# Optimization experiments

Hardware: AMD Instinct MI355X
Metric: run time of the kernel (lower is better)

## Reference

```python
import jax, jax.numpy as jnp
import numpy as np

N = 50000   # nodes
E = 800000  # edges
B = 64      # graphs in batch
IN = 128    # in_features
HID = 64    # hidden_channels
H = 4       # head_count
C = 10      # out_classes
NEG = 0.2   # leaky relu negative slope
EPS = 1e-5  # batchnorm eps (eval mode, running mean 0 / var 1)


def _gat(x, edge_index, W, a_src, a_dst, b):
    """PyG GATConv (add_self_loops=False, concat=True), eval mode (no dropout)."""
    Hh, F = a_src.shape
    xW = (x @ W).reshape(-1, Hh, F)                       # [N,H,F]
    src, dst = edge_index[0], edge_index[1]
    e = (jnp.einsum('nhf,hf->nh', xW, a_src)[src]
         + jnp.einsum('nhf,hf->nh', xW, a_dst)[dst])      # [E,H]
    e = jnp.where(e > 0, e, NEG * e)                      # leaky relu
    m = jax.ops.segment_max(e, dst, num_segments=N)       # per-dst max
    m = jnp.where(jnp.isfinite(m), m, 0.0)
    p = jnp.exp(e - m[dst])
    denom = jax.ops.segment_sum(p, dst, num_segments=N)
    alpha = p / jnp.maximum(denom[dst], 1e-16)            # edge softmax over dst
    out = jax.ops.segment_sum(alpha[:, :, None] * xW[src], dst, num_segments=N)
    return out.reshape(-1, Hh * F) + b


def _bn_relu(y, g, be):
    # BatchNorm1d in eval mode with running_mean=0, running_var=1, then ReLU
    return jax.nn.relu(g * y / jnp.sqrt(1.0 + EPS) + be)


def setup_inputs():
    key = jax.random.key(0)
    ks = jax.random.split(key, 24)
    s = lambda k, shape: (jax.random.normal(k, shape, jnp.float32) * 0.05)
    z = lambda shape: jnp.zeros(shape, jnp.float32)
    o = lambda shape: jnp.ones(shape, jnp.float32)
    return {
        'acc_flag': 0,
        'x': jax.random.normal(ks[0], (N, IN), jnp.float32),
        'edge_index': jax.random.randint(ks[1], (2, E), 0, N),
        'batch': jnp.sort(jax.random.randint(ks[2], (N,), 0, B)),
        # layer 1: GATConv(IN -> HID, heads=H, concat)
        'W1': s(ks[3], (IN, H * HID)), 'a_src1': s(ks[4], (H, HID)), 'a_dst1': s(ks[5], (H, HID)), 'b1': z((H * HID,)),
        # proj: GATConv(H*HID -> HID, heads=1) + BN
        'W2': s(ks[6], (H * HID, HID)), 'a_src2': s(ks[7], (1, HID)), 'a_dst2': s(ks[8], (1, HID)), 'b2': z((HID,)), 'g2': o((HID,)), 'be2': z((HID,)),
        # block 1
        'W3': s(ks[9], (HID, HID)), 'a_src3': s(ks[10], (1, HID)), 'a_dst3': s(ks[11], (1, HID)), 'b3': z((HID,)), 'g3': o((HID,)), 'be3': z((HID,)),
        # block 2
        'W4': s(ks[12], (HID, HID)), 'a_src4': s(ks[13], (1, HID)), 'a_dst4': s(ks[14], (1, HID)), 'b4': z((HID,)), 'g4': o((HID,)), 'be4': z((HID,)),
        # MLP head
        'Wh1': s(ks[15], (HID, 128)), 'bh1': z((128,)),
        'Wh2': s(ks[16], (128, C)), 'bh2': z((C,)),
    }


def reference(acc_flag, x, edge_index, batch,
              W1, a_src1, a_dst1, b1,
              W2, a_src2, a_dst2, b2, g2, be2,
              W3, a_src3, a_dst3, b3, g3, be3,
              W4, a_src4, a_dst4, b4, g4, be4,
              Wh1, bh1, Wh2, bh2):
    # hardware GAT layer + ReLU (relu applied twice in original -> idempotent)
    x1 = jax.nn.relu(_gat(x, edge_index, W1, a_src1, a_dst1, b1))   # [N, H*HID]
    # projection block: residual base is zeros (shape mismatch H*HID vs HID)
    h = _bn_relu(_gat(x1, edge_index, W2, a_src2, a_dst2, b2), g2, be2)
    # residual blocks (shapes match -> x + relu(bn(y)))
    h = h + _bn_relu(_gat(h, edge_index, W3, a_src3, a_dst3, b3), g3, be3)
    h = h + _bn_relu(_gat(h, edge_index, W4, a_src4, a_dst4, b4), g4, be4)
    # global mean pool over graphs
    pooled = jax.ops.segment_sum(h, batch, num_segments=B)
    cnt = jnp.maximum(jax.ops.segment_sum(jnp.ones((N,), h.dtype), batch, num_segments=B), 1.0)
    hp = pooled / cnt[:, None]                                      # [B, HID]
    # MLP head
    return jax.nn.relu(hp @ Wh1 + bh1) @ Wh2 + bh2                  # [B, C]
```

## Files before the change

### kernel.cpp

```cpp
#include <hip/hip_runtime.h>

#define N_NODES 50000
#define N_EDGES 800000
#define N_GRAPHS 64
#define NEG_SLOPE 0.2f
#define BN_RSQ 0.9999950000374997f
#define NB_SCAN ((N_NODES + 255) / 256)

typedef __bf16 bf16x8 __attribute__((ext_vector_type(8)));
typedef float floatx4 __attribute__((ext_vector_type(4)));

__device__ __forceinline__ float lrelu(float v) { return v > 0.0f ? v : NEG_SLOPE * v; }

__device__ __forceinline__ float b2f(unsigned short u) {
    return __uint_as_float(((unsigned int)u) << 16);
}
__device__ __forceinline__ unsigned short f2b(float f) {
    unsigned int u = __float_as_uint(f);
    return (unsigned short)((u + 0x7fffu + ((u >> 16) & 1u)) >> 16);
}
__device__ __forceinline__ float blo(unsigned int d) { return __uint_as_float(d << 16); }
__device__ __forceinline__ float bhi(unsigned int d) { return __uint_as_float(d & 0xffff0000u); }

__global__ void k_prep(const int* __restrict__ ei, int* __restrict__ deg,
                       const float* __restrict__ W1, const float* __restrict__ W2,
                       const float* __restrict__ W3, const float* __restrict__ W4,
                       unsigned short* __restrict__ Wt1, unsigned short* __restrict__ Wt2,
                       unsigned short* __restrict__ Wt3, unsigned short* __restrict__ Wt4) {
    int i = blockIdx.x * 256 + threadIdx.x;
    if (i < 32768) {
        int k = i >> 8, n = i & 255;
        Wt1[n * 128 + k] = f2b(W1[i]);
    } else if (i < 49152) {
        int j = i - 32768;
        int k = j >> 6, n = j & 63;
        Wt2[n * 256 + k] = f2b(W2[j]);
    } else if (i < 53248) {
        int j = i - 49152;
        int k = j >> 6, n = j & 63;
        Wt3[n * 64 + k] = f2b(W3[j]);
    } else if (i < 57344) {
        int j = i - 53248;
        int k = j >> 6, n = j & 63;
        Wt4[n * 64 + k] = f2b(W4[j]);
    }
    if (i < N_EDGES) atomicAdd(&deg[ei[N_EDGES + i]], 1);
}

__global__ __launch_bounds__(256) void k_offs(const int* __restrict__ deg, int* __restrict__ offs,
                                              int* __restrict__ total, const int* __restrict__ batch,
                                              int* __restrict__ bounds, int* __restrict__ bh) {
    __shared__ int lh[64];
    if (threadIdx.x < 64) lh[threadIdx.x] = 0;
    __syncthreads();
    if (blockIdx.x == 0 && threadIdx.x <= N_GRAPHS) {
        int g = threadIdx.x;
        int lo = 0, hi = N_NODES;
        while (lo < hi) {
            int mid = (lo + hi) >> 1;
            if (batch[mid] < g) lo = mid + 1; else hi = mid;
        }
        bounds[g] = lo;
    }
    int i = blockIdx.x * blockDim.x + threadIdx.x;
    int lane = threadIdx.x & 63;
    int v = (i < N_NODES) ? deg[i] : 0;
    int incl = v;
    for (int o = 1; o < 64; o <<= 1) {
        int t = __shfl_up(incl, o);
        if (lane >= o) incl += t;
    }
    int wtot = __shfl(incl, 63);
    int base = 0;
    if (lane == 0) base = atomicAdd(total, wtot);
    base = __shfl(base, 0);
    if (i < N_NODES) {
        offs[i] = base + incl - v;
        atomicAdd(&lh[63 - min(v, 63)], 1);
    }
    __syncthreads();
    if (threadIdx.x < 64) bh[blockIdx.x * 64 + threadIdx.x] = lh[threadIdx.x];
}

__global__ __launch_bounds__(256) void k_pscan(const int* __restrict__ bh, int* __restrict__ bb) {
    __shared__ int partial[4][64];
    __shared__ int bbase[64];
    const int tid = threadIdx.x;
    const int b = tid & 63, q = tid >> 6;
    const int per = (NB_SCAN + 3) / 4;
    const int k0 = q * per, k1 = min(k0 + per, NB_SCAN);
    int s = 0;
    for (int k = k0; k < k1; ++k) s += bh[k * 64 + b];
    partial[q][b] = s;
    __syncthreads();
    if (tid < 64) {
        int tot = partial[0][tid] + partial[1][tid] + partial[2][tid] + partial[3][tid];
        int incl = tot;
        for (int o = 1; o < 64; o <<= 1) {
            int t2 = __shfl_up(incl, o);
            if (tid >= o) incl += t2;
        }
        bbase[tid] = incl - tot;
    }
    __syncthreads();
    int run = bbase[b];
    for (int q2 = 0; q2 < q; ++q2) run += partial[q2][b];
    for (int k = k0; k < k1; ++k) {
        bb[k * 64 + b] = run;
        run += bh[k * 64 + b];
    }
}

__global__ __launch_bounds__(256) void k_fillperm(const int* __restrict__ ei,
                                                  const int* __restrict__ offs,
                                                  int* __restrict__ cur, int* __restrict__ csr_src,
                                                  const int* __restrict__ deg,
                                                  const int* __restrict__ bb,
                                                  int* __restrict__ perm) {
    __shared__ int lcnt[64];
    if (blockIdx.x < NB_SCAN) {
        if (threadIdx.x < 64) lcnt[threadIdx.x] = 0;
        __syncthreads();
        int i = blockIdx.x * 256 + threadIdx.x;
        if (i < N_NODES) {
            int b = 63 - min(deg[i], 63);
            int r = atomicAdd(&lcnt[b], 1);
            perm[bb[blockIdx.x * 64 + b] + r] = i;
        }
    }
    int e = blockIdx.x * 256 + threadIdx.x;
    if (e < N_EDGES) {
        int d = ei[N_EDGES + e];
        int pos = offs[d] + atomicAdd(&cur[d], 1);
        csr_src[pos] = ei[e];
    }
}

template <int K, int N, int HEADS, bool AF32>
__global__ __launch_bounds__(256) void k_mgemm(const void* __restrict__ Ap,
                                               const unsigned short* __restrict__ Bt,
                                               const float* __restrict__ asrc,
                                               const float* __restrict__ adst,
                                               unsigned short* __restrict__ out,
                                               float* __restrict__ es,
                                               float* __restrict__ ed, int rows) {
    constexpr int LDP = K + 8;
    __shared__ unsigned short As[64 * LDP];
    const int tid = threadIdx.x;
    const int r0 = blockIdx.x * 64;
    if (AF32) {
        const float* A = (const float*)Ap;
        for (int i = tid; i < 16 * K; i += 256) {
            int r = i / (K / 4), c4 = i % (K / 4);
            int row = r0 + r;
            float4 v = (row < rows) ? *(const float4*)&A[(size_t)row * K + c4 * 4]
                                    : make_float4(0.f, 0.f, 0.f, 0.f);
            ushort4 u;
            u.x = f2b(v.x); u.y = f2b(v.y); u.z = f2b(v.z); u.w = f2b(v.w);
            *(ushort4*)&As[r * LDP + c4 * 4] = u;
        }
    } else {
        const unsigned short* A = (const unsigned short*)Ap;
        for (int i = tid; i < 8 * K; i += 256) {
            int r = i / (K / 8), c8 = i % (K / 8);
            int row = r0 + r;
            uint4 v;
            if (row < rows) v = *(const uint4*)&A[(size_t)row * K + c8 * 8];
            else { v.x = v.y = v.z = v.w = 0; }
            *(uint4*)&As[r * LDP + c8 * 8] = v;
        }
    }
    __syncthreads();
    const int w = tid >> 6, lane = tid & 63;
    const int quad = lane >> 4, l16 = lane & 15;
    const int gr0 = r0 + w * 16 + quad * 4;
    bf16x8 afrag[K / 32];
#pragma unroll
    for (int kk = 0; kk < K / 32; ++kk)
        afrag[kk] = *(const bf16x8*)&As[(w * 16 + l16) * LDP + kk * 32 + quad * 8];
    float sacc[4] = {0.f, 0.f, 0.f, 0.f};
    float dacc[4] = {0.f, 0.f, 0.f, 0.f};
#pragma unroll 1
    for (int ct = 0; ct < N / 16; ++ct) {
        floatx4 acc = {0.f, 0.f, 0.f, 0.f};
#pragma unroll
        for (int kk = 0; kk < K / 32; ++kk) {
            const bf16x8 bfrag =
                *(const bf16x8*)&Bt[(size_t)(ct * 16 + l16) * K + kk * 32 + quad * 8];
            acc = __builtin_amdgcn_mfma_f32_16x16x32_bf16(afrag[kk], bfrag, acc, 0, 0, 0);
        }
        const int gc = ct * 16 + l16;
        const int hh = gc >> 6;
        const int f = gc & 63;
        const float as = asrc[hh * 64 + f];
        const float ad = adst[hh * 64 + f];
#pragma unroll
        for (int rg = 0; rg < 4; ++rg) {
            sacc[rg] = fmaf(acc[rg], as, sacc[rg]);
            dacc[rg] = fmaf(acc[rg], ad, dacc[rg]);
        }
#pragma unroll
        for (int rg = 0; rg < 4; ++rg) {
            int gr = gr0 + rg;
            if (gr < rows) out[(size_t)gr * N + gc] = f2b(acc[rg]);
        }
        if ((ct & 3) == 3) {
#pragma unroll
            for (int rg = 0; rg < 4; ++rg) {
                float s = sacc[rg], d = dacc[rg];
                for (int o = 1; o < 16; o <<= 1) {
                    s += __shfl_xor(s, o);
                    d += __shfl_xor(d, o);
                }
                if (l16 == 0) {
                    int gr = gr0 + rg;
                    if (gr < rows) {
                        es[(size_t)gr * HEADS + hh] = s;
                        ed[(size_t)gr * HEADS + hh] = d;
                    }
                }
                sacc[rg] = 0.f;
                dacc[rg] = 0.f;
            }
        }
    }
}

__global__ __launch_bounds__(256) void k_gat1(
    const unsigned short* __restrict__ xW, const float* __restrict__ es, const float* __restrict__ ed,
    const int* __restrict__ offs, const int* __restrict__ deg, const int* __restrict__ csr,
    const int* __restrict__ perm, const float* __restrict__ bias, unsigned short* __restrict__ out) {
    __shared__ float ps[4][4 * 68];
    __shared__ int sbuf[4][64];
    const int wv = threadIdx.x >> 6;
    const int lane = threadIdx.x & 63;
    const int grp = lane >> 4, t = lane & 15;
    const int h = t >> 2;
    const int pidx = blockIdx.x * 16 + wv * 4 + grp;
    const int n = perm[pidx];
    const int off = offs[n];
    const int dg = deg[n];
    const float4 edv = *(const float4*)&ed[n * 4];
    const int cb = t * 16;

    float acc[16];
#pragma unroll
    for (int k = 0; k < 16; ++k) acc[k] = 0.f;
    float dsum = 0.f;

    for (int base = 0; base < dg; base += 16) {
        const int idx = base + t;
        int s_l = 0;
        float p0 = 0.f, p1 = 0.f, p2 = 0.f, p3 = 0.f;
        if (idx < dg) {
            s_l = csr[off + idx];
            const float4 ev = *(const float4*)&es[s_l * 4];
            p0 = __expf(lrelu(ev.x + edv.x));
            p1 = __expf(lrelu(ev.y + edv.y));
            p2 = __expf(lrelu(ev.z + edv.z));
            p3 = __expf(lrelu(ev.w + edv.w));
        }
        *(float4*)&ps[wv][grp * 68 + t * 4] = make_float4(p0, p1, p2, p3);
        sbuf[wv][grp * 16 + t] = s_l;
        const int cnt = min(16, dg - base);
        const int cntR = (cnt + 3) & ~3;
        for (int j = 0; j < cntR; j += 4) {
            const float pa = ps[wv][grp * 68 + (j + 0) * 4 + h];
            const float pb = ps[wv][grp * 68 + (j + 1) * 4 + h];
            const float pc = ps[wv][grp * 68 + (j + 2) * 4 + h];
            const float pd = ps[wv][grp * 68 + (j + 3) * 4 + h];
            const int sa = sbuf[wv][grp * 16 + j + 0];
            const int sb = sbuf[wv][grp * 16 + j + 1];
            const int sc = sbuf[wv][grp * 16 + j + 2];
            const int sd = sbuf[wv][grp * 16 + j + 3];
            const uint4 a0 = *(const uint4*)&xW[(size_t)sa * 256 + cb];
            const uint4 a1 = *(const uint4*)&xW[(size_t)sa * 256 + cb + 8];
            const uint4 b0 = *(const uint4*)&xW[(size_t)sb * 256 + cb];
            const uint4 b1 = *(const uint4*)&xW[(size_t)sb * 256 + cb + 8];
            const uint4 c0 = *(const uint4*)&xW[(size_t)sc * 256 + cb];
            const uint4 c1 = *(const uint4*)&xW[(size_t)sc * 256 + cb + 8];
            const uint4 d0 = *(const uint4*)&xW[(size_t)sd * 256 + cb];
            const uint4 d1 = *(const uint4*)&xW[(size_t)sd * 256 + cb + 8];
            dsum += (pa + pb) + (pc + pd);
            acc[0]  = fmaf(pa, blo(a0.x), acc[0]);
            acc[1]  = fmaf(pa, bhi(a0.x), acc[1]);
            acc[2]  = fmaf(pa, blo(a0.y), acc[2]);
            acc[3]  = fmaf(pa, bhi(a0.y), acc[3]);
            acc[4]  = fmaf(pa, blo(a0.z), acc[4]);
            acc[5]  = fmaf(pa, bhi(a0.z), acc[5]);
            acc[6]  = fmaf(pa, blo(a0.w), acc[6]);
            acc[7]  = fmaf(pa, bhi(a0.w), acc[7]);
            acc[8]  = fmaf(pa, blo(a1.x), acc[8]);
            acc[9]  = fmaf(pa, bhi(a1.x), acc[9]);
            acc[10] = fmaf(pa, blo(a1.y), acc[10]);
            acc[11] = fmaf(pa, bhi(a1.y), acc[11]);
            acc[12] = fmaf(pa, blo(a1.z), acc[12]);
            acc[13] = fmaf(pa, bhi(a1.z), acc[13]);
            acc[14] = fmaf(pa, blo(a1.w), acc[14]);
            acc[15] = fmaf(pa, bhi(a1.w), acc[15]);
            acc[0]  = fmaf(pb, blo(b0.x), acc[0]);
            acc[1]  = fmaf(pb, bhi(b0.x), acc[1]);
            acc[2]  = fmaf(pb, blo(b0.y), acc[2]);
            acc[3]  = fmaf(pb, bhi(b0.y), acc[3]);
            acc[4]  = fmaf(pb, blo(b0.z), acc[4]);
            acc[5]  = fmaf(pb, bhi(b0.z), acc[5]);
            acc[6]  = fmaf(pb, blo(b0.w), acc[6]);
            acc[7]  = fmaf(pb, bhi(b0.w), acc[7]);
            acc[8]  = fmaf(pb, blo(b1.x), acc[8]);
            acc[9]  = fmaf(pb, bhi(b1.x), acc[9]);
            acc[10] = fmaf(pb, blo(b1.y), acc[10]);
            acc[11] = fmaf(pb, bhi(b1.y), acc[11]);
            acc[12] = fmaf(pb, blo(b1.z), acc[12]);
            acc[13] = fmaf(pb, bhi(b1.z), acc[13]);
            acc[14] = fmaf(pb, blo(b1.w), acc[14]);
            acc[15] = fmaf(pb, bhi(b1.w), acc[15]);
            acc[0]  = fmaf(pc, blo(c0.x), acc[0]);
            acc[1]  = fmaf(pc, bhi(c0.x), acc[1]);
            acc[2]  = fmaf(pc, blo(c0.y), acc[2]);
            acc[3]  = fmaf(pc, bhi(c0.y), acc[3]);
            acc[4]  = fmaf(pc, blo(c0.z), acc[4]);
            acc[5]  = fmaf(pc, bhi(c0.z), acc[5]);
            acc[6]  = fmaf(pc, blo(c0.w), acc[6]);
            acc[7]  = fmaf(pc, bhi(c0.w), acc[7]);
            acc[8]  = fmaf(pc, blo(c1.x), acc[8]);
            acc[9]  = fmaf(pc, bhi(c1.x), acc[9]);
            acc[10] = fmaf(pc, blo(c1.y), acc[10]);
            acc[11] = fmaf(pc, bhi(c1.y), acc[11]);
            acc[12] = fmaf(pc, blo(c1.z), acc[12]);
            acc[13] = fmaf(pc, bhi(c1.z), acc[13]);
            acc[14] = fmaf(pc, blo(c1.w), acc[14]);
            acc[15] = fmaf(pc, bhi(c1.w), acc[15]);
            acc[0]  = fmaf(pd, blo(d0.x), acc[0]);
            acc[1]  = fmaf(pd, bhi(d0.x), acc[1]);
            acc[2]  = fmaf(pd, blo(d0.y), acc[2]);
            acc[3]  = fmaf(pd, bhi(d0.y), acc[3]);
            acc[4]  = fmaf(pd, blo(d0.z), acc[4]);
            acc[5]  = fmaf(pd, bhi(d0.z), acc[5]);
            acc[6]  = fmaf(pd, blo(d0.w), acc[6]);
            acc[7]  = fmaf(pd, bhi(d0.w), acc[7]);
            acc[8]  = fmaf(pd, blo(d1.x), acc[8]);
            acc[9]  = fmaf(pd, bhi(d1.x), acc[9]);
            acc[10] = fmaf(pd, blo(d1.y), acc[10]);
            acc[11] = fmaf(pd, bhi(d1.y), acc[11]);
            acc[12] = fmaf(pd, blo(d1.z), acc[12]);
            acc[13] = fmaf(pd, bhi(d1.z), acc[13]);
            acc[14] = fmaf(pd, blo(d1.w), acc[14]);
            acc[15] = fmaf(pd, bhi(d1.w), acc[15]);
        }
    }
    const float inv = 1.0f / fmaxf(dsum, 1e-16f);
#pragma unroll
    for (int k4 = 0; k4 < 16; k4 += 4) {
        const int c = cb + k4;
        const float4 bv = *(const float4*)&bias[c];
        ushort4 o4;
        o4.x = f2b(fmaxf(fmaf(acc[k4 + 0], inv, bv.x), 0.f));
        o4.y = f2b(fmaxf(fmaf(acc[k4 + 1], inv, bv.y), 0.f));
        o4.z = f2b(fmaxf(fmaf(acc[k4 + 2], inv, bv.z), 0.f));
        o4.w = f2b(fmaxf(fmaf(acc[k4 + 3], inv, bv.w), 0.f));
        *(ushort4*)&out[(size_t)n * 256 + c] = o4;
    }
}

template <bool RES>
__global__ __launch_bounds__(256) void k_gatL(
    const unsigned short* __restrict__ xW, const float* __restrict__ es, const float* __restrict__ ed,
    const int* __restrict__ offs, const int* __restrict__ deg, const int* __restrict__ csr,
    const int* __restrict__ perm, const float* __restrict__ bias, const float* __restrict__ gam,
    const float* __restrict__ bet, float* __restrict__ h, unsigned short* __restrict__ hb) {
    __shared__ float ps[4][64];
    __shared__ int sbuf[4][64];
    const int wv = threadIdx.x >> 6;
    const int lane = threadIdx.x & 63;
    const int grp = lane >> 3, t = lane & 7;
    const int pidx = blockIdx.x * 32 + wv * 8 + grp;
    if (pidx >= N_NODES) return;
    const int n = perm[pidx];
    const int off = offs[n];
    const int dg = deg[n];
    const float edn = ed[n];
    const int cb = t * 8;

    float acc[8];
#pragma unroll
    for (int k = 0; k < 8; ++k) acc[k] = 0.f;
    float dsum = 0.f;

    for (int base = 0; base < dg; base += 8) {
        const int idx = base + t;
        int s_l = 0;
        float p_l = 0.f;
        if (idx < dg) {
            s_l = csr[off + idx];
            p_l = __expf(lrelu(es[s_l] + edn));
        }
        ps[wv][grp * 8 + t] = p_l;
        sbuf[wv][grp * 8 + t] = s_l;
        const int cnt = min(8, dg - base);
        const int cntR = (cnt + 3) & ~3;
        for (int j = 0; j < cntR; j += 4) {
            const float pa = ps[wv][grp * 8 + j + 0];
            const float pb = ps[wv][grp * 8 + j + 1];
            const float pc = ps[wv][grp * 8 + j + 2];
            const float pd = ps[wv][grp * 8 + j + 3];
            const int sa = sbuf[wv][grp * 8 + j + 0];
            const int sb = sbuf[wv][grp * 8 + j + 1];
            const int sc = sbuf[wv][grp * 8 + j + 2];
            const int sd = sbuf[wv][grp * 8 + j + 3];
            const uint4 a = *(const uint4*)&xW[(size_t)sa * 64 + cb];
            const uint4 b = *(const uint4*)&xW[(size_t)sb * 64 + cb];
            const uint4 c = *(const uint4*)&xW[(size_t)sc * 64 + cb];
            const uint4 d = *(const uint4*)&xW[(size_t)sd * 64 + cb];
            dsum += (pa + pb) + (pc + pd);
            acc[0] = fmaf(pa, blo(a.x), acc[0]);
            acc[1] = fmaf(pa, bhi(a.x), acc[1]);
            acc[2] = fmaf(pa, blo(a.y), acc[2]);
            acc[3] = fmaf(pa, bhi(a.y), acc[3]);
            acc[4] = fmaf(pa, blo(a.z), acc[4]);
            acc[5] = fmaf(pa, bhi(a.z), acc[5]);
            acc[6] = fmaf(pa, blo(a.w), acc[6]);
            acc[7] = fmaf(pa, bhi(a.w), acc[7]);
            acc[0] = fmaf(pb, blo(b.x), acc[0]);
            acc[1] = fmaf(pb, bhi(b.x), acc[1]);
            acc[2] = fmaf(pb, blo(b.y), acc[2]);
            acc[3] = fmaf(pb, bhi(b.y), acc[3]);
            acc[4] = fmaf(pb, blo(b.z), acc[4]);
            acc[5] = fmaf(pb, bhi(b.z), acc[5]);
            acc[6] = fmaf(pb, blo(b.w), acc[6]);
            acc[7] = fmaf(pb, bhi(b.w), acc[7]);
            acc[0] = fmaf(pc, blo(c.x), acc[0]);
            acc[1] = fmaf(pc, bhi(c.x), acc[1]);
            acc[2] = fmaf(pc, blo(c.y), acc[2]);
            acc[3] = fmaf(pc, bhi(c.y), acc[3]);
            acc[4] = fmaf(pc, blo(c.z), acc[4]);
            acc[5] = fmaf(pc, bhi(c.z), acc[5]);
            acc[6] = fmaf(pc, blo(c.w), acc[6]);
            acc[7] = fmaf(pc, bhi(c.w), acc[7]);
            acc[0] = fmaf(pd, blo(d.x), acc[0]);
            acc[1] = fmaf(pd, bhi(d.x), acc[1]);
            acc[2] = fmaf(pd, blo(d.y), acc[2]);
            acc[3] = fmaf(pd, bhi(d.y), acc[3]);
            acc[4] = fmaf(pd, blo(d.z), acc[4]);
            acc[5] = fmaf(pd, bhi(d.z), acc[5]);
            acc[6] = fmaf(pd, blo(d.w), acc[6]);
            acc[7] = fmaf(pd, bhi(d.w), acc[7]);
        }
    }
    const float inv = 1.0f / fmaxf(dsum, 1e-16f);
    float hn[8];
#pragma unroll
    for (int k = 0; k < 8; ++k) {
        const int c = cb + k;
        const float y = fmaf(acc[k], inv, bias[c]);
        const float z = fmaxf(fmaf(gam[c] * y, BN_RSQ, bet[c]), 0.f);
        hn[k] = RES ? h[(size_t)n * 64 + c] + z : z;
    }
    *(float4*)&h[(size_t)n * 64 + cb] = make_float4(hn[0], hn[1], hn[2], hn[3]);
    *(float4*)&h[(size_t)n * 64 + cb + 4] = make_float4(hn[4], hn[5], hn[6], hn[7]);
    ushort4 u0, u1;
    u0.x = f2b(hn[0]); u0.y = f2b(hn[1]); u0.z = f2b(hn[2]); u0.w = f2b(hn[3]);
    u1.x = f2b(hn[4]); u1.y = f2b(hn[5]); u1.z = f2b(hn[6]); u1.w = f2b(hn[7]);
    *(ushort4*)&hb[(size_t)n * 64 + cb] = u0;
    *(ushort4*)&hb[(size_t)n * 64 + cb + 4] = u1;
}

__global__ __launch_bounds__(256) void k_pool2(const float* __restrict__ h,
                                               const int* __restrict__ bounds,
                                               float* __restrict__ hp) {
    __shared__ float part[4][64];
    const int g = blockIdx.x;
    const int lane = threadIdx.x & 63;
    const int wid = threadIdx.x >> 6;
    const int s = bounds[g], e = bounds[g + 1];
    float acc = 0.f;
    for (int n = s + wid; n < e; n += 4) acc += h[n * 64 + lane];
    part[wid][lane] = acc;
    __syncthreads();
    if (wid == 0) {
        float v = part[0][lane] + part[1][lane] + part[2][lane] + part[3][lane];
        hp[g * 64 + lane] = v / fmaxf((float)(e - s), 1.0f);
    }
}

__global__ __launch_bounds__(256) void k_head(const float* __restrict__ hpg,
                                              const float* __restrict__ Wh1,
                                              const float* __restrict__ bh1,
                                              const float* __restrict__ Wh2,
                                              const float* __restrict__ bh2,
                                              float* __restrict__ out) {
    __shared__ float hp[64 * 64];
    __shared__ float t1[64 * 128];
    const int tid = threadIdx.x;
    for (int i = tid; i < 64 * 64; i += 256) hp[i] = hpg[i];
    __syncthreads();
    for (int i = tid; i < 64 * 128; i += 256) {
        int g = i >> 7, j = i & 127;
        float s = bh1[j];
        for (int k = 0; k < 64; ++k) s = fmaf(hp[g * 64 + k], Wh1[k * 128 + j], s);
        t1[i] = fmaxf(s, 0.f);
    }
    __syncthreads();
    for (int i = tid; i < 640; i += 256) {
        int g = i / 10, j = i - g * 10;
        float s = bh2[j];
        for (int k = 0; k < 128; ++k) s = fmaf(t1[g * 128 + k], Wh2[k * 10 + j], s);
        out[i] = s;
    }
}

extern "C" void kernel_launch(void* const* d_in, const int* in_sizes, int n_in,
                              void* d_out, int out_size, void* d_ws, size_t ws_size,
                              hipStream_t stream) {
    const float* x = (const float*)d_in[1];
    const int* ei = (const int*)d_in[2];
    const int* batch = (const int*)d_in[3];
    const float* W1 = (const float*)d_in[4];
    const float* a_src1 = (const float*)d_in[5];
    const float* a_dst1 = (const float*)d_in[6];
    const float* b1 = (const float*)d_in[7];
    const float* W2 = (const float*)d_in[8];
    const float* a_src2 = (const float*)d_in[9];
    const float* a_dst2 = (const float*)d_in[10];
    const float* b2 = (const float*)d_in[11];
    const float* g2 = (const float*)d_in[12];
    const float* be2 = (const float*)d_in[13];
    const float* W3 = (const float*)d_in[14];
    const float* a_src3 = (const float*)d_in[15];
    const float* a_dst3 = (const float*)d_in[16];
    const float* b3 = (const float*)d_in[17];
    const float* g3 = (const float*)d_in[18];
    const float* be3 = (const float*)d_in[19];
    const float* W4 = (const float*)d_in[20];
    const float* a_src4 = (const float*)d_in[21];
    const float* a_dst4 = (const float*)d_in[22];
    const float* b4 = (const float*)d_in[23];
    const float* g4 = (const float*)d_in[24];
    const float* be4 = (const float*)d_in[25];
    const float* Wh1 = (const float*)d_in[26];
    const float* bh1 = (const float*)d_in[27];
    const float* Wh2 = (const float*)d_in[28];
    const float* bh2 = (const float*)d_in[29];
    float* out = (float*)d_out;

    char* p = (char*)d_ws;
    auto alloc = [&](size_t bytes) {
        void* r = (void*)p;
        p += (bytes + 255) & ~(size_t)255;
        return r;
    };
    unsigned short* bufA = (unsigned short*)alloc((size_t)N_NODES * 256 * 2);
    unsigned short* x1b = (unsigned short*)alloc((size_t)N_NODES * 256 * 2);
    float* h = (float*)alloc((size_t)N_NODES * 64 * 4);
    unsigned short* hb = (unsigned short*)alloc((size_t)N_NODES * 64 * 2);
    float* es1 = (float*)alloc((size_t)N_NODES * 4 * 4);
    float* ed1 = (float*)alloc((size_t)N_NODES * 4 * 4);
    float* esL = (float*)alloc((size_t)N_NODES * 4);
    float* edL = (float*)alloc((size_t)N_NODES * 4);
    int* offs = (int*)alloc((size_t)N_NODES * 4);
    int* csr = (int*)alloc((size_t)N_EDGES * 4);
    int* perm = (int*)alloc((size_t)N_NODES * 4);
    int* bounds = (int*)alloc((size_t)(N_GRAPHS + 1) * 4);
    int* bh_hist = (int*)alloc((size_t)NB_SCAN * 64 * 4);
    int* bb = (int*)alloc((size_t)NB_SCAN * 64 * 4);
    float* hpool = (float*)alloc((size_t)N_GRAPHS * 64 * 4);
    unsigned short* Wt1 = (unsigned short*)alloc((size_t)128 * 256 * 2);
    unsigned short* Wt2 = (unsigned short*)alloc((size_t)256 * 64 * 2);
    unsigned short* Wt3 = (unsigned short*)alloc((size_t)64 * 64 * 2);
    unsigned short* Wt4 = (unsigned short*)alloc((size_t)64 * 64 * 2);
    char* z0 = p;
    int* deg = (int*)alloc((size_t)N_NODES * 4);
    int* cur = (int*)alloc((size_t)N_NODES * 4);
    int* total = (int*)alloc(256);
    size_t zbytes = (size_t)(p - z0);
    hipMemsetAsync(z0, 0, zbytes, stream);

    const int edgeBlocks = (N_EDGES + 255) / 256;
    const int mgemmBlocks = (N_NODES + 63) / 64;
    const int gat1Blocks = (N_NODES + 15) / 16;
    const int gatLBlocks = (N_NODES + 31) / 32;

    k_prep<<<edgeBlocks, 256, 0, stream>>>(ei, deg, W1, W2, W3, W4, Wt1, Wt2, Wt3, Wt4);

    k_offs<<<NB_SCAN, 256, 0, stream>>>(deg, offs, total, batch, bounds, bh_hist);
    k_pscan<<<1, 256, 0, stream>>>(bh_hist, bb);
    k_fillperm<<<edgeBlocks, 256, 0, stream>>>(ei, offs, cur, csr, deg, bb, perm);

    k_mgemm<128, 256, 4, true><<<mgemmBlocks, 256, 0, stream>>>(x, Wt1, a_src1, a_dst1,
                                                                bufA, es1, ed1, N_NODES);
    k_gat1<<<gat1Blocks, 256, 0, stream>>>(bufA, es1, ed1, offs, deg, csr, perm, b1, x1b);

    k_mgemm<256, 64, 1, false><<<mgemmBlocks, 256, 0, stream>>>(x1b, Wt2, a_src2, a_dst2,
                                                                bufA, esL, edL, N_NODES);
    k_gatL<false><<<gatLBlocks, 256, 0, stream>>>(bufA, esL, edL, offs, deg, csr, perm, b2, g2, be2, h, hb);

    k_mgemm<64, 64, 1, false><<<mgemmBlocks, 256, 0, stream>>>(hb, Wt3, a_src3, a_dst3,
                                                               bufA, esL, edL, N_NODES);
    k_gatL<true><<<gatLBlocks, 256, 0, stream>>>(bufA, esL, edL, offs, deg, csr, perm, b3, g3, be3, h, hb);

    k_mgemm<64, 64, 1, false><<<mgemmBlocks, 256, 0, stream>>>(hb, Wt4, a_src4, a_dst4,
                                                               bufA, esL, edL, N_NODES);
    k_gatL<true><<<gatLBlocks, 256, 0, stream>>>(bufA, esL, edL, offs, deg, csr, perm, b4, g4, be4, h, hb);

    k_pool2<<<N_GRAPHS, 256, 0, stream>>>(h, bounds, hpool);
    k_head<<<1, 256, 0, stream>>>(hpool, Wh1, bh1, Wh2, bh2, out);
}
```

Before: 522.0 us.

## Pair nodes from both ends of degree order in GAT1; batch 8 gathers in gatL

Each 16-lane group in k_gat1 now processes two nodes, one at position g0 and one at N-1-g0 of the degree-sorted permutation, with half as many blocks launched. This pairs high-degree with low-degree nodes to balance per-group work and reduce tail imbalance. In k_gatL the inner loop now loads all 8 staged neighbours' rows at once instead of groups of 4, raising memory-level parallelism. Padded entries carry p=0, so the extra loads only cost bandwidth, at the price of more registers. The pairing relies on N_NODES being even.

```diff
diff --git a/kernel.cpp b/kernel.cpp
--- a/kernel.cpp
+++ b/kernel.cpp
@@ -236,129 +236,135 @@
     const int lane = threadIdx.x & 63;
     const int grp = lane >> 4, t = lane & 15;
     const int h = t >> 2;
-    const int pidx = blockIdx.x * 16 + wv * 4 + grp;
-    const int n = perm[pidx];
-    const int off = offs[n];
-    const int dg = deg[n];
-    const float4 edv = *(const float4*)&ed[n * 4];
+    const int g0 = blockIdx.x * 16 + wv * 4 + grp;
+    if (g0 >= N_NODES / 2) return;
     const int cb = t * 16;
 
-    float acc[16];
-#pragma unroll
-    for (int k = 0; k < 16; ++k) acc[k] = 0.f;
-    float dsum = 0.f;
-
-    for (int base = 0; base < dg; base += 16) {
-        const int idx = base + t;
-        int s_l = 0;
-        float p0 = 0.f, p1 = 0.f, p2 = 0.f, p3 = 0.f;
-        if (idx < dg) {
-            s_l = csr[off + idx];
-            const float4 ev = *(const float4*)&es[s_l * 4];
-            p0 = __expf(lrelu(ev.x + edv.x));
-            p1 = __expf(lrelu(ev.y + edv.y));
-            p2 = __expf(lrelu(ev.z + edv.z));
-            p3 = __expf(lrelu(ev.w + edv.w));
-        }
-        *(float4*)&ps[wv][grp * 68 + t * 4] = make_float4(p0, p1, p2, p3);
-        sbuf[wv][grp * 16 + t] = s_l;
-        const int cnt = min(16, dg - base);
-        const int cntR = (cnt + 3) & ~3;
-        for (int j = 0; j < cntR; j += 4) {
-            const float pa = ps[wv][grp * 68 + (j + 0) * 4 + h];
-            const float pb = ps[wv][grp * 68 + (j + 1) * 4 + h];
-            const float pc = ps[wv][grp * 68 + (j + 2) * 4 + h];
-            const float pd = ps[wv][grp * 68 + (j + 3) * 4 + h];
-            const int sa = sbuf[wv][grp * 16 + j + 0];
-            const int sb = sbuf[wv][grp * 16 + j + 1];
-            const int sc = sbuf[wv][grp * 16 + j + 2];
-            const int sd = sbuf[wv][grp * 16 + j + 3];
-            const uint4 a0 = *(const uint4*)&xW[(size_t)sa * 256 + cb];
-            const uint4 a1 = *(const uint4*)&xW[(size_t)sa * 256 + cb + 8];
-            const uint4 b0 = *(const uint4*)&xW[(size_t)sb * 256 + cb];
-            const uint4 b1 = *(const uint4*)&xW[(size_t)sb * 256 + cb + 8];
-            const uint4 c0 = *(const uint4*)&xW[(size_t)sc * 256 + cb];
-            const uint4 c1 = *(const uint4*)&xW[(size_t)sc * 256 + cb + 8];
-            const uint4 d0 = *(const uint4*)&xW[(size_t)sd * 256 + cb];
-            const uint4 d1 = *(const uint4*)&xW[(size_t)sd * 256 + cb + 8];
-            dsum += (pa + pb) + (pc + pd);
-            acc[0]  = fmaf(pa, blo(a0.x), acc[0]);
-            acc[1]  = fmaf(pa, bhi(a0.x), acc[1]);
-            acc[2]  = fmaf(pa, blo(a0.y), acc[2]);
-            acc[3]  = fmaf(pa, bhi(a0.y), acc[3]);
-            acc[4]  = fmaf(pa, blo(a0.z), acc[4]);
-            acc[5]  = fmaf(pa, bhi(a0.z), acc[5]);
-            acc[6]  = fmaf(pa, blo(a0.w), acc[6]);
-            acc[7]  = fmaf(pa, bhi(a0.w), acc[7]);
-            acc[8]  = fmaf(pa, blo(a1.x), acc[8]);
-            acc[9]  = fmaf(pa, bhi(a1.x), acc[9]);
-            acc[10] = fmaf(pa, blo(a1.y), acc[10]);
-            acc[11] = fmaf(pa, bhi(a1.y), acc[11]);
-            acc[12] = fmaf(pa, blo(a1.z), acc[12]);
-            acc[13] = fmaf(pa, bhi(a1.z), acc[13]);
-            acc[14] = fmaf(pa, blo(a1.w), acc[14]);
-            acc[15] = fmaf(pa, bhi(a1.w), acc[15]);
-            acc[0]  = fmaf(pb, blo(b0.x), acc[0]);
-            acc[1]  = fmaf(pb, bhi(b0.x), acc[1]);
-            acc[2]  = fmaf(pb, blo(b0.y), acc[2]);
-            acc[3]  = fmaf(pb, bhi(b0.y), acc[3]);
-            acc[4]  = fmaf(pb, blo(b0.z), acc[4]);
-            acc[5]  = fmaf(pb, bhi(b0.z), acc[5]);
-            acc[6]  = fmaf(pb, blo(b0.w), acc[6]);
-            acc[7]  = fmaf(pb, bhi(b0.w), acc[7]);
-            acc[8]  = fmaf(pb, blo(b1.x), acc[8]);
-            acc[9]  = fmaf(pb, bhi(b1.x), acc[9]);
-            acc[10] = fmaf(pb, blo(b1.y), acc[10]);
-            acc[11] = fmaf(pb, bhi(b1.y), acc[11]);
-            acc[12] = fmaf(pb, blo(b1.z), acc[12]);
-            acc[13] = fmaf(pb, bhi(b1.z), acc[13]);
-            acc[14] = fmaf(pb, blo(b1.w), acc[14]);
-            acc[15] = fmaf(pb, bhi(b1.w), acc[15]);
-            acc[0]  = fmaf(pc, blo(c0.x), acc[0]);
-            acc[1]  = fmaf(pc, bhi(c0.x), acc[1]);
-            acc[2]  = fmaf(pc, blo(c0.y), acc[2]);
-            acc[3]  = fmaf(pc, bhi(c0.y), acc[3]);
-            acc[4]  = fmaf(pc, blo(c0.z), acc[4]);
-            acc[5]  = fmaf(pc, bhi(c0.z), acc[5]);
-            acc[6]  = fmaf(pc, blo(c0.w), acc[6]);
-            acc[7]  = fmaf(pc, bhi(c0.w), acc[7]);
-            acc[8]  = fmaf(pc, blo(c1.x), acc[8]);
-            acc[9]  = fmaf(pc, bhi(c1.x), acc[9]);
-            acc[10] = fmaf(pc, blo(c1.y), acc[10]);
-            acc[11] = fmaf(pc, bhi(c1.y), acc[11]);
-            acc[12] = fmaf(pc, blo(c1.z), acc[12]);
-            acc[13] = fmaf(pc, bhi(c1.z), acc[13]);
-            acc[14] = fmaf(pc, blo(c1.w), acc[14]);
-            acc[15] = fmaf(pc, bhi(c1.w), acc[15]);
-            acc[0]  = fmaf(pd, blo(d0.x), acc[0]);
-            acc[1]  = fmaf(pd, bhi(d0.x), acc[1]);
-            acc[2]  = fmaf(pd, blo(d0.y), acc[2]);
-            acc[3]  = fmaf(pd, bhi(d0.y), acc[3]);
-            acc[4]  = fmaf(pd, blo(d0.z), acc[4]);
-            acc[5]  = fmaf(pd, bhi(d0.z), acc[5]);
-            acc[6]  = fmaf(pd, blo(d0.w), acc[6]);
-            acc[7]  = fmaf(pd, bhi(d0.w), acc[7]);
-            acc[8]  = fmaf(pd, blo(d1.x), acc[8]);
-            acc[9]  = fmaf(pd, bhi(d1.x), acc[9]);
-            acc[10] = fmaf(pd, blo(d1.y), acc[10]);
-            acc[11] = fmaf(pd, bhi(d1.y), acc[11]);
-            acc[12] = fmaf(pd, blo(d1.z), acc[12]);
-            acc[13] = fmaf(pd, bhi(d1.z), acc[13]);
-            acc[14] = fmaf(pd, blo(d1.w), acc[14]);
-            acc[15] = fmaf(pd, bhi(d1.w), acc[15]);
-        }
-    }
-    const float inv = 1.0f / fmaxf(dsum, 1e-16f);
-#pragma unroll
-    for (int k4 = 0; k4 < 16; k4 += 4) {
-        const int c = cb + k4;
-        const float4 bv = *(const float4*)&bias[c];
-        ushort4 o4;
-        o4.x = f2b(fmaxf(fmaf(acc[k4 + 0], inv, bv.x), 0.f));
-        o4.y = f2b(fmaxf(fmaf(acc[k4 + 1], inv, bv.y), 0.f));
-        o4.z = f2b(fmaxf(fmaf(acc[k4 + 2], inv, bv.z), 0.f));
-        o4.w = f2b(fmaxf(fmaf(acc[k4 + 3], inv, bv.w), 0.f));
-        *(ushort4*)&out[(size_t)n * 256 + c] = o4;
+#pragma unroll 1
+    for (int half = 0; half < 2; ++half) {
+        const int pidx = half ? (N_NODES - 1 - g0) : g0;
+        const int n = perm[pidx];
+        const int off = offs[n];
+        const int dg = deg[n];
+        const float4 edv = *(const float4*)&ed[n * 4];
+
+        float acc[16];
+#pragma unroll
+        for (int k = 0; k < 16; ++k) acc[k] = 0.f;
+        float dsum = 0.f;
+
+        for (int base = 0; base < dg; base += 16) {
+            const int idx = base + t;
+            int s_l = 0;
+            float p0 = 0.f, p1 = 0.f, p2 = 0.f, p3 = 0.f;
+            if (idx < dg) {
+                s_l = csr[off + idx];
+                const float4 ev = *(const float4*)&es[s_l * 4];
+                p0 = __expf(lrelu(ev.x + edv.x));
+                p1 = __expf(lrelu(ev.y + edv.y));
+                p2 = __expf(lrelu(ev.z + edv.z));
+                p3 = __expf(lrelu(ev.w + edv.w));
+            }
+            *(float4*)&ps[wv][grp * 68 + t * 4] = make_float4(p0, p1, p2, p3);
+            sbuf[wv][grp * 16 + t] = s_l;
+            const int cnt = min(16, dg - base);
+            const int cntR = (cnt + 3) & ~3;
+            for (int j = 0; j < cntR; j += 4) {
+                const float pa = ps[wv][grp * 68 + (j + 0) * 4 + h];
+                const float pb = ps[wv][grp * 68 + (j + 1) * 4 + h];
+                const float pc = ps[wv][grp * 68 + (j + 2) * 4 + h];
+                const float pd = ps[wv][grp * 68 + (j + 3) * 4 + h];
+                const int sa = sbuf[wv][grp * 16 + j + 0];
+                const int sb = sbuf[wv][grp * 16 + j + 1];
+                const int sc = sbuf[wv][grp * 16 + j + 2];
+                const int sd = sbuf[wv][grp * 16 + j + 3];
+                const uint4 a0 = *(const uint4*)&xW[(size_t)sa * 256 + cb];
+                const uint4 a1 = *(const uint4*)&xW[(size_t)sa * 256 + cb + 8];
+                const uint4 b0 = *(const uint4*)&xW[(size_t)sb * 256 + cb];
+                const uint4 b1 = *(const uint4*)&xW[(size_t)sb * 256 + cb + 8];
+                const uint4 c0 = *(const uint4*)&xW[(size_t)sc * 256 + cb];
+                const uint4 c1 = *(const uint4*)&xW[(size_t)sc * 256 + cb + 8];
+                const uint4 d0 = *(const uint4*)&xW[(size_t)sd * 256 + cb];
+                const uint4 d1 = *(const uint4*)&xW[(size_t)sd * 256 + cb + 8];
+                dsum += (pa + pb) + (pc + pd);
+                acc[0]  = fmaf(pa, blo(a0.x), acc[0]);
+                acc[1]  = fmaf(pa, bhi(a0.x), acc[1]);
+                acc[2]  = fmaf(pa, blo(a0.y), acc[2]);
+                acc[3]  = fmaf(pa, bhi(a0.y), acc[3]);
+                acc[4]  = fmaf(pa, blo(a0.z), acc[4]);
+                acc[5]  = fmaf(pa, bhi(a0.z), acc[5]);
+                acc[6]  = fmaf(pa, blo(a0.w), acc[6]);
+                acc[7]  = fmaf(pa, bhi(a0.w), acc[7]);
+                acc[8]  = fmaf(pa, blo(a1.x), acc[8]);
+                acc[9]  = fmaf(pa, bhi(a1.x), acc[9]);
+                acc[10] = fmaf(pa, blo(a1.y), acc[10]);
+                acc[11] = fmaf(pa, bhi(a1.y), acc[11]);
+                acc[12] = fmaf(pa, blo(a1.z), acc[12]);
+                acc[13] = fmaf(pa, bhi(a1.z), acc[13]);
+                acc[14] = fmaf(pa, blo(a1.w), acc[14]);
+                acc[15] = fmaf(pa, bhi(a1.w), acc[15]);
+                acc[0]  = fmaf(pb, blo(b0.x), acc[0]);
+                acc[1]  = fmaf(pb, bhi(b0.x), acc[1]);
+                acc[2]  = fmaf(pb, blo(b0.y), acc[2]);
+                acc[3]  = fmaf(pb, bhi(b0.y), acc[3]);
+                acc[4]  = fmaf(pb, blo(b0.z), acc[4]);
+                acc[5]  = fmaf(pb, bhi(b0.z), acc[5]);
+                acc[6]  = fmaf(pb, blo(b0.w), acc[6]);
+                acc[7]  = fmaf(pb, bhi(b0.w), acc[7]);
+                acc[8]  = fmaf(pb, blo(b1.x), acc[8]);
+                acc[9]  = fmaf(pb, bhi(b1.x), acc[9]);
+                acc[10] = fmaf(pb, blo(b1.y), acc[10]);
+                acc[11] = fmaf(pb, bhi(b1.y), acc[11]);
+                acc[12] = fmaf(pb, blo(b1.z), acc[12]);
+                acc[13] = fmaf(pb, bhi(b1.z), acc[13]);
+                acc[14] = fmaf(pb, blo(b1.w), acc[14]);
+                acc[15] = fmaf(pb, bhi(b1.w), acc[15]);
+                acc[0]  = fmaf(pc, blo(c0.x), acc[0]);
+                acc[1]  = fmaf(pc, bhi(c0.x), acc[1]);
+                acc[2]  = fmaf(pc, blo(c0.y), acc[2]);
+                acc[3]  = fmaf(pc, bhi(c0.y), acc[3]);
+                acc[4]  = fmaf(pc, blo(c0.z), acc[4]);
+                acc[5]  = fmaf(pc, bhi(c0.z), acc[5]);
+                acc[6]  = fmaf(pc, blo(c0.w), acc[6]);
+                acc[7]  = fmaf(pc, bhi(c0.w), acc[7]);
+                acc[8]  = fmaf(pc, blo(c1.x), acc[8]);
+                acc[9]  = fmaf(pc, bhi(c1.x), acc[9]);
+                acc[10] = fmaf(pc, blo(c1.y), acc[10]);
+                acc[11] = fmaf(pc, bhi(c1.y), acc[11]);
+                acc[12] = fmaf(pc, blo(c1.z), acc[12]);
+                acc[13] = fmaf(pc, bhi(c1.z), acc[13]);
+                acc[14] = fmaf(pc, blo(c1.w), acc[14]);
+                acc[15] = fmaf(pc, bhi(c1.w), acc[15]);
+                acc[0]  = fmaf(pd, blo(d0.x), acc[0]);
+                acc[1]  = fmaf(pd, bhi(d0.x), acc[1]);
+                acc[2]  = fmaf(pd, blo(d0.y), acc[2]);
+                acc[3]  = fmaf(pd, bhi(d0.y), acc[3]);
+                acc[4]  = fmaf(pd, blo(d0.z), acc[4]);
+                acc[5]  = fmaf(pd, bhi(d0.z), acc[5]);
+                acc[6]  = fmaf(pd, blo(d0.w), acc[6]);
+                acc[7]  = fmaf(pd, bhi(d0.w), acc[7]);
+                acc[8]  = fmaf(pd, blo(d1.x), acc[8]);
+                acc[9]  = fmaf(pd, bhi(d1.x), acc[9]);
+                acc[10] = fmaf(pd, blo(d1.y), acc[10]);
+                acc[11] = fmaf(pd, bhi(d1.y), acc[11]);
+                acc[12] = fmaf(pd, blo(d1.z), acc[12]);
+                acc[13] = fmaf(pd, bhi(d1.z), acc[13]);
+                acc[14] = fmaf(pd, blo(d1.w), acc[14]);
+                acc[15] = fmaf(pd, bhi(d1.w), acc[15]);
+            }
+        }
+        const float inv = 1.0f / fmaxf(dsum, 1e-16f);
+#pragma unroll
+        for (int k4 = 0; k4 < 16; k4 += 4) {
+            const int c = cb + k4;
+            const float4 bv = *(const float4*)&bias[c];
+            ushort4 o4;
+            o4.x = f2b(fmaxf(fmaf(acc[k4 + 0], inv, bv.x), 0.f));
+            o4.y = f2b(fmaxf(fmaf(acc[k4 + 1], inv, bv.y), 0.f));
+            o4.z = f2b(fmaxf(fmaf(acc[k4 + 2], inv, bv.z), 0.f));
+            o4.w = f2b(fmaxf(fmaf(acc[k4 + 3], inv, bv.w), 0.f));
+            *(ushort4*)&out[(size_t)n * 256 + c] = o4;
+        }
     }
 }
 
@@ -396,54 +402,27 @@
         }
         ps[wv][grp * 8 + t] = p_l;
         sbuf[wv][grp * 8 + t] = s_l;
-        const int cnt = min(8, dg - base);
-        const int cntR = (cnt + 3) & ~3;
-        for (int j = 0; j < cntR; j += 4) {
-            const float pa = ps[wv][grp * 8 + j + 0];
-            const float pb = ps[wv][grp * 8 + j + 1];
-            const float pc = ps[wv][grp * 8 + j + 2];
-            const float pd = ps[wv][grp * 8 + j + 3];
-            const int sa = sbuf[wv][grp * 8 + j + 0];
-            const int sb = sbuf[wv][grp * 8 + j + 1];
-            const int sc = sbuf[wv][grp * 8 + j + 2];
-            const int sd = sbuf[wv][grp * 8 + j + 3];
-            const uint4 a = *(const uint4*)&xW[(size_t)sa * 64 + cb];
-            const uint4 b = *(const uint4*)&xW[(size_t)sb * 64 + cb];
-            const uint4 c = *(const uint4*)&xW[(size_t)sc * 64 + cb];
-            const uint4 d = *(const uint4*)&xW[(size_t)sd * 64 + cb];
-            dsum += (pa + pb) + (pc + pd);
-            acc[0] = fmaf(pa, blo(a.x), acc[0]);
-            acc[1] = fmaf(pa, bhi(a.x), acc[1]);
-            acc[2] = fmaf(pa, blo(a.y), acc[2]);
-            acc[3] = fmaf(pa, bhi(a.y), acc[3]);
-            acc[4] = fmaf(pa, blo(a.z), acc[4]);
-            acc[5] = fmaf(pa, bhi(a.z), acc[5]);
-            acc[6] = fmaf(pa, blo(a.w), acc[6]);
-            acc[7] = fmaf(pa, bhi(a.w), acc[7]);
-            acc[0] = fmaf(pb, blo(b.x), acc[0]);
-            acc[1] = fmaf(pb, bhi(b.x), acc[1]);
-            acc[2] = fmaf(pb, blo(b.y), acc[2]);
-            acc[3] = fmaf(pb, bhi(b.y), acc[3]);
-            acc[4] = fmaf(pb, blo(b.z), acc[4]);
-            acc[5] = fmaf(pb, bhi(b.z), acc[5]);
-            acc[6] = fmaf(pb, blo(b.w), acc[6]);
-            acc[7] = fmaf(pb, bhi(b.w), acc[7]);
-            acc[0] = fmaf(pc, blo(c.x), acc[0]);
-            acc[1] = fmaf(pc, bhi(c.x), acc[1]);
-            acc[2] = fmaf(pc, blo(c.y), acc[2]);
-            acc[3] = fmaf(pc, bhi(c.y), acc[3]);
-            acc[4] = fmaf(pc, blo(c.z), acc[4]);
-            acc[5] = fmaf(pc, bhi(c.z), acc[5]);
-            acc[6] = fmaf(pc, blo(c.w), acc[6]);
-            acc[7] = fmaf(pc, bhi(c.w), acc[7]);
-            acc[0] = fmaf(pd, blo(d.x), acc[0]);
-            acc[1] = fmaf(pd, bhi(d.x), acc[1]);
-            acc[2] = fmaf(pd, blo(d.y), acc[2]);
-            acc[3] = fmaf(pd, bhi(d.y), acc[3]);
-            acc[4] = fmaf(pd, blo(d.z), acc[4]);
-            acc[5] = fmaf(pd, bhi(d.z), acc[5]);
-            acc[6] = fmaf(pd, blo(d.w), acc[6]);
-            acc[7] = fmaf(pd, bhi(d.w), acc[7]);
+        float pp[8];
+        int ss[8];
+#pragma unroll
+        for (int q = 0; q < 8; ++q) {
+            pp[q] = ps[wv][grp * 8 + q];
+            ss[q] = sbuf[wv][grp * 8 + q];
+        }
+        uint4 u[8];
+#pragma unroll
+        for (int q = 0; q < 8; ++q) u[q] = *(const uint4*)&xW[(size_t)ss[q] * 64 + cb];
+#pragma unroll
+        for (int q = 0; q < 8; ++q) {
+            dsum += pp[q];
+            acc[0] = fmaf(pp[q], blo(u[q].x), acc[0]);
+            acc[1] = fmaf(pp[q], bhi(u[q].x), acc[1]);
+            acc[2] = fmaf(pp[q], blo(u[q].y), acc[2]);
+            acc[3] = fmaf(pp[q], bhi(u[q].y), acc[3]);
+            acc[4] = fmaf(pp[q], blo(u[q].z), acc[4]);
+            acc[5] = fmaf(pp[q], bhi(u[q].z), acc[5]);
+            acc[6] = fmaf(pp[q], blo(u[q].w), acc[6]);
+            acc[7] = fmaf(pp[q], bhi(u[q].w), acc[7]);
         }
     }
     const float inv = 1.0f / fmaxf(dsum, 1e-16f);
@@ -576,7 +555,7 @@
 
     const int edgeBlocks = (N_EDGES + 255) / 256;
     const int mgemmBlocks = (N_NODES + 63) / 64;
-    const int gat1Blocks = (N_NODES + 15) / 16;
+    const int gat1Blocks = (N_NODES / 2 + 15) / 16;
     const int gatLBlocks = (N_NODES + 31) / 32;
 
     k_prep<<<edgeBlocks, 256, 0, stream>>>(ei, deg, W1, W2, W3, W4, Wt1, Wt2, Wt3, Wt4);
```

Result: no change. 523.6 us (+0.3%).
